# Performance work log

Measured on AMD Instinct MI355X. Metric: run time of the kernel, lower is better.

Reference implementation:

```python
import jax, jax.numpy as jnp
import numpy as np

N_EMBED = 1024
CUTOFFS = [20000, 60000, 180000]
N_VOCAB = 267735
BOUNDS = [0] + CUTOFFS + [N_VOCAB]            # cluster boundaries
N_EMBEDS = [1024, 256, 64, 16]                # n_embed / 4**i
N_TOK = 1024
N_CLUSTERS = len(CUTOFFS)                      # 3 tail clusters


def setup_inputs() -> dict:
    key = jax.random.key(0)
    ks = jax.random.split(key, 12)

    def w(k, shape):
        fan_in = shape[0]
        return (jax.random.normal(k, shape, jnp.float32) / np.sqrt(fan_in)).astype(jnp.float32)

    inp = {}
    inp["hidden"] = jax.random.normal(ks[0], (N_TOK, N_EMBED), jnp.float32)
    inp["target"] = jax.random.randint(ks[1], (N_TOK,), 0, N_VOCAB)
    # head: layers[0] = Linear(n_embed, cutoffs[0]); clusters = Linear(n_embed, n_clusters)
    inp["W_head"] = w(ks[2], (N_EMBED, BOUNDS[1]))
    inp["b_head"] = jnp.zeros((BOUNDS[1],), jnp.float32)
    inp["W_cluster"] = w(ks[3], (N_EMBED, N_CLUSTERS))
    inp["b_cluster"] = jnp.zeros((N_CLUSTERS,), jnp.float32)
    # tails: projections[i-1] = Linear(n_embed, n_embeds[i], bias=False); layers[i] = Linear(n_embeds[i], end-start)
    for i in range(1, N_CLUSTERS + 1):
        size = BOUNDS[i + 1] - BOUNDS[i]
        inp[f"W_proj{i}"] = w(ks[3 + 2 * i], (N_EMBED, N_EMBEDS[i]))
        inp[f"W_tail{i}"] = w(ks[4 + 2 * i], (N_EMBEDS[i], size))
        inp[f"b_tail{i}"] = jnp.zeros((size,), jnp.float32)
    return inp


def _adaptive_nll(hidden, target, W_head, b_head, W_cluster, b_cluster, tails):
    # head logits = [vocab cluster 0 | cluster logits], then log_softmax (matches torch.cat + log_softmax)
    head_logit = jnp.concatenate(
        [hidden @ W_head + b_head, hidden @ W_cluster + b_cluster], axis=1)  # [N, cut0 + n_clusters]
    head_lp = jax.nn.log_softmax(head_logit, axis=1)

    # cluster 0: logprob = head_lp[n, target]
    t0 = jnp.clip(target, 0, BOUNDS[1] - 1)
    lp0 = jnp.take_along_axis(head_lp, t0[:, None], axis=1)[:, 0]
    nll = jnp.where(target < BOUNDS[1], -lp0, jnp.zeros((), head_lp.dtype))

    # tail clusters i=1..3: logprob = head_lp[:, -i] + tail_log_softmax[n, target-start]
    for i, (Wp, Wt, bt) in enumerate(tails, start=1):
        start, end = BOUNDS[i], BOUNDS[i + 1]
        tail_lp = jax.nn.log_softmax((hidden @ Wp) @ Wt + bt, axis=1)  # [N, end-start]
        rel = jnp.clip(target - start, 0, end - start - 1)
        lp_i = head_lp[:, -i] + jnp.take_along_axis(tail_lp, rel[:, None], axis=1)[:, 0]
        in_bucket = (target >= start) & (target < end)
        nll = jnp.where(in_bucket, -lp_i, nll)
    return nll  # [N], per-token negative log-likelihood (keep_order=True semantics)


def reference(hidden, target, W_head, b_head, W_cluster, b_cluster,
              W_proj1, W_tail1, b_tail1,
              W_proj2, W_tail2, b_tail2,
              W_proj3, W_tail3, b_tail3):
    tails = [(W_proj1, W_tail1, b_tail1),
             (W_proj2, W_tail2, b_tail2),
             (W_proj3, W_tail3, b_tail3)]
    return _adaptive_nll(hidden, target, W_head, b_head, W_cluster, b_cluster, tails)
```

## Files before the change

kernel.cpp:

```cpp
#include <hip/hip_runtime.h>
#include <cstdint>
#include <cstddef>


typedef unsigned short u16;
typedef __attribute__((ext_vector_type(8))) __bf16 bf16x8;
typedef __attribute__((ext_vector_type(8))) u16 u16x8;
typedef __attribute__((ext_vector_type(4))) float f32x4;

#define AS1 __attribute__((address_space(1)))
#define AS3 __attribute__((address_space(3)))

__device__ __forceinline__ u16 f2bf(float f){
  union { float f; unsigned u; } v; v.f = f;
  unsigned r = v.u + 0x7fffu + ((v.u >> 16) & 1u);
  return (u16)(r >> 16);
}
__device__ __forceinline__ void glds16(const void* g, void* l){
  __builtin_amdgcn_global_load_lds((AS1 unsigned*)(uintptr_t)g,
                                   (AS3 unsigned*)(unsigned)(uintptr_t)l, 16, 0, 0);
}

__global__ void k_cvt_hidden(const float* __restrict__ h, u16* __restrict__ a0,
                             int* __restrict__ cnt, int* __restrict__ trel){
  int g = blockIdx.x * 256 + threadIdx.x;
  if (g < 4096) trel[g] = -1;
  if (g < 4) cnt[g] = 0;
  int i = g * 8;
  f32x4 v0 = *(const f32x4*)(h + i);
  f32x4 v1 = *(const f32x4*)(h + i + 4);
  u16x8 o;
  o[0]=f2bf(v0.x); o[1]=f2bf(v0.y); o[2]=f2bf(v0.z); o[3]=f2bf(v0.w);
  o[4]=f2bf(v1.x); o[5]=f2bf(v1.y); o[6]=f2bf(v1.z); o[7]=f2bf(v1.w);
  *(u16x8*)(a0 + i) = o;
}

__global__ void k_compact(const int* __restrict__ tgt, int* __restrict__ cnt,
                          int* __restrict__ idx1, int* __restrict__ idx2,
                          int* __restrict__ idx3, int* __restrict__ pos,
                          int* __restrict__ tr0, int* __restrict__ tr1,
                          int* __restrict__ tr2, int* __restrict__ tr3){
  int n = blockIdx.x * 256 + threadIdx.x;
  int t = tgt[n];
  int p = 0;
  tr0[n] = (t < 20000) ? t : -1;
  if (t >= 20000){
    int b = (t < 60000) ? 0 : (t < 180000 ? 1 : 2);
    p = atomicAdd(&cnt[b], 1);
    if (b == 0){ idx1[p] = n; tr1[p] = t - 20000; }
    else if (b == 1){ idx2[p] = n; tr2[p] = t - 60000; }
    else { idx3[p] = n; tr3[p] = t - 180000; }
  }
  pos[n] = p;
}

__global__ void k_gather(const int* __restrict__ cnt,
                         const int* __restrict__ idx1, const int* __restrict__ idx2,
                         const int* __restrict__ idx3,
                         const u16* __restrict__ A1, const u16* __restrict__ A2,
                         const u16* __restrict__ A3,
                         u16* __restrict__ A1c, u16* __restrict__ A2c,
                         u16* __restrict__ A3c){
  int u = blockIdx.x * 256 + threadIdx.x;
  const u16* src; u16* dst;
  if (u < 32768){
    int r = u >> 5, c = u & 31;
    if (r >= cnt[0]) return;
    src = A1 + (size_t)idx1[r] * 256 + c * 8;
    dst = A1c + (size_t)r * 256 + c * 8;
  } else if (u < 40960){
    int v = u - 32768; int r = v >> 3, c = v & 7;
    if (r >= cnt[1]) return;
    src = A2 + (size_t)idx2[r] * 64 + c * 8;
    dst = A2c + (size_t)r * 64 + c * 8;
  } else {
    int v = u - 40960; int r = v >> 2, c = v & 3;
    if (r >= cnt[2]) return;
    src = A3 + (size_t)idx3[r] * 32 + c * 8;
    dst = A3c + (size_t)r * 32 + c * 8;
  }
  *(u16x8*)dst = *(const u16x8*)src;
}

struct TJob { const float* W; u16* BT; int K, N, Kpad, nrows, nx, base, blk; };
struct TJobs { TJob j[8]; int nj; };

__global__ void k_transpose_multi(TJobs jobs){
  int id = blockIdx.x;
  int ji = 0;
  #pragma unroll
  for (int i = 1; i < 8; ++i)
    if (i < jobs.nj && id >= jobs.j[i].base) ji = i;
  TJob jb = jobs.j[ji];
  int local = id - jb.base;
  int bx = local % jb.nx;
  int by = local / jb.nx;

  __shared__ float t[64][65];
  const int n0 = bx * 64;
  const int k0 = by * 64;
  const bool al = (jb.N & 3) == 0;
  for (int i = threadIdx.x; i < 64*16; i += 256){
    int r = i >> 4, c4 = (i & 15) * 4;
    int k = k0 + r, n = n0 + c4;
    f32x4 v; v.x=0.f; v.y=0.f; v.z=0.f; v.w=0.f;
    if (k < jb.K){
      if (al && n + 3 < jb.N) v = *(const f32x4*)(jb.W + (size_t)k * jb.N + n);
      else { for (int q = 0; q < 4; ++q) if (n + q < jb.N) v[q] = jb.W[(size_t)k * jb.N + n + q]; }
    }
    t[r][c4] = v.x; t[r][c4+1] = v.y; t[r][c4+2] = v.z; t[r][c4+3] = v.w;
  }
  __syncthreads();
  for (int i = threadIdx.x; i < 64*8; i += 256){
    int rn = i >> 3, c8 = (i & 7) * 8;
    int n = n0 + rn;
    if (k0 + c8 < jb.Kpad && n < jb.nrows){
      u16x8 o;
      #pragma unroll
      for (int q = 0; q < 8; ++q) o[q] = f2bf(t[c8 + q][rn]);
      size_t off;
      if (jb.blk)
        off = (((size_t)(n >> 7) * (jb.Kpad >> 6) + (k0 >> 6)) * 128 + (n & 127)) * 64 + c8;
      else
        off = (size_t)n * jb.Kpad + k0 + c8;
      *(u16x8*)(jb.BT + off) = o;
    }
  }
}

__global__ __launch_bounds__(512)
void k_proj_gemm(const u16* __restrict__ A, const u16* __restrict__ BT,
                 const float* __restrict__ bc,
                 u16* __restrict__ A1, u16* __restrict__ A2,
                 u16* __restrict__ A3, float* __restrict__ cl)
{
  constexpr int BK = 64, K = 1024;
  __shared__ u16 As[256 * BK];
  __shared__ u16 Bs[128 * BK];
  const int tid  = threadIdx.x;
  const int lane = tid & 63, wid = tid >> 6;
  const int wm = wid & 3, wn = wid >> 2;
  const int l15 = lane & 15, l4 = lane >> 4;
  const int m0 = blockIdx.y * 256;
  const int n0 = blockIdx.x * 128;

  f32x4 acc[4][4];
  #pragma unroll
  for (int m = 0; m < 4; ++m)
    #pragma unroll
    for (int n = 0; n < 4; ++n){ acc[m][n].x=0.f; acc[m][n].y=0.f; acc[m][n].z=0.f; acc[m][n].w=0.f; }

  for (int kt = 0; kt < K / BK; ++kt){
    #pragma unroll
    for (int i = 0; i < 4; ++i){
      int c = wid * 4 + i;
      int row = c * 8 + lane / 8, kb = lane % 8;
      glds16((const char*)(A + (size_t)(m0 + row) * K + kt * BK) + kb * 16,
             (char*)As + c * 1024);
    }
    #pragma unroll
    for (int i = 0; i < 2; ++i){
      int c = wid * 2 + i;
      int row = c * 8 + lane / 8, kb = lane % 8;
      glds16((const char*)(BT + (size_t)(n0 + row) * K + kt * BK) + kb * 16,
             (char*)Bs + c * 1024);
    }
    __syncthreads();
    #pragma unroll
    for (int ks = 0; ks < 2; ++ks){
      bf16x8 af[4], bfr[4];
      #pragma unroll
      for (int m = 0; m < 4; ++m)
        af[m] = *(const bf16x8*)((const char*)As + (wm*64 + m*16 + l15) * (BK*2) + ks*64 + l4*16);
      #pragma unroll
      for (int n = 0; n < 4; ++n)
        bfr[n] = *(const bf16x8*)((const char*)Bs + (wn*64 + n*16 + l15) * (BK*2) + ks*64 + l4*16);
      #pragma unroll
      for (int m = 0; m < 4; ++m)
        #pragma unroll
        for (int n = 0; n < 4; ++n)
          acc[m][n] = __builtin_amdgcn_mfma_f32_16x16x32_bf16(af[m], bfr[n], acc[m][n], 0, 0, 0);
    }
    __syncthreads();
  }
  #pragma unroll
  for (int m = 0; m < 4; ++m)
    #pragma unroll
    for (int n = 0; n < 4; ++n)
      #pragma unroll
      for (int q = 0; q < 4; ++q){
        int c = n0 + wn*64 + n*16 + l15;
        int r = m0 + wm*64 + m*16 + l4*4 + q;
        float v = acc[m][n][q];
        if (c < 256)      A1[(size_t)r*256 + c] = f2bf(v);
        else if (c < 320) A2[(size_t)r*64 + (c-256)] = f2bf(v);
        else if (c < 336){ u16* p = A3 + (size_t)r*32 + (c-320);
                           p[0] = f2bf(v); p[16] = 0; }
        else if (c < 339) cl[(size_t)r*3 + (c-336)] = v + bc[c-336];
      }
}

__global__ __launch_bounds__(512)
void k_gemm_lse256(const u16* __restrict__ A, const u16* __restrict__ BT,
                   const float* __restrict__ bias, int K, int N,
                   float* __restrict__ P, int ntiles,
                   const int* __restrict__ cntp, int bucket,
                   const int* __restrict__ tgt_rel, const int* __restrict__ rowmap,
                   float* __restrict__ tl)
{
  constexpr int BK = 64;
  if (cntp && (int)(blockIdx.y * 256) >= cntp[bucket]) return;
  __shared__ u16 As[256 * BK];
  __shared__ u16 Bs[128 * BK];
  __shared__ float reds[2][256];
  __shared__ int trel_s[256];

  const int tid  = threadIdx.x;
  const int lane = tid & 63, wid = tid >> 6;
  const int wm = wid & 3, wn = wid >> 2;
  const int l15 = lane & 15, l4 = lane >> 4;
  const int m0 = blockIdx.y * 256;
  const int n0 = blockIdx.x * 128;
  const int srow = lane >> 3, skb = lane & 7;

  if (tid < 256) trel_s[tid] = tgt_rel[m0 + tid];

  f32x4 acc[4][4];
  #pragma unroll
  for (int m = 0; m < 4; ++m)
    #pragma unroll
    for (int n = 0; n < 4; ++n){ acc[m][n].x=0.f; acc[m][n].y=0.f; acc[m][n].z=0.f; acc[m][n].w=0.f; }

  const int ksteps = K / BK;
  for (int kt = 0; kt < ksteps; ++kt){
    #pragma unroll
    for (int i = 0; i < 4; ++i){
      int c = wid * 4 + i;
      int row = c * 8 + srow;
      int kbs = skb ^ (row & 7);
      glds16((const char*)(A + (size_t)(m0 + row) * K + kt * BK) + kbs * 16,
             (char*)As + c * 1024);
    }
    #pragma unroll
    for (int i = 0; i < 2; ++i){
      int c = wid * 2 + i;
      int row = c * 8 + srow;
      int kbs = skb ^ (row & 7);
      glds16((const char*)(BT + ((size_t)(blockIdx.x * ksteps + kt) * 128 + row) * 64) + kbs * 16,
             (char*)Bs + c * 1024);
    }
    __syncthreads();
    #pragma unroll
    for (int ks = 0; ks < 2; ++ks){
      bf16x8 af[4], bfr[4];
      #pragma unroll
      for (int m = 0; m < 4; ++m){
        int r = wm*64 + m*16 + l15;
        af[m] = *(const bf16x8*)((const char*)As + r*128 + (((ks*4 + l4) ^ (r & 7)) * 16));
      }
      #pragma unroll
      for (int n = 0; n < 4; ++n){
        int r = wn*64 + n*16 + l15;
        bfr[n] = *(const bf16x8*)((const char*)Bs + r*128 + (((ks*4 + l4) ^ (r & 7)) * 16));
      }
      #pragma unroll
      for (int m = 0; m < 4; ++m)
        #pragma unroll
        for (int n = 0; n < 4; ++n)
          acc[m][n] = __builtin_amdgcn_mfma_f32_16x16x32_bf16(af[m], bfr[n], acc[m][n], 0, 0, 0);
    }
    __syncthreads();
  }

  float bv[4]; bool val[4];
  #pragma unroll
  for (int n = 0; n < 4; ++n){
    int col = n0 + wn*64 + n*16 + l15;
    val[n] = col < N;
    bv[n] = val[n] ? bias[col] : 0.f;
  }
  #pragma unroll
  for (int m = 0; m < 4; ++m)
    #pragma unroll
    for (int q = 0; q < 4; ++q){
      int lrow = wm*64 + m*16 + l4*4 + q;
      int tr = trel_s[lrow];
      float Sl = 0.f;
      #pragma unroll
      for (int n = 0; n < 4; ++n){
        if (val[n]){
          float lg = acc[m][n][q] + bv[n];
          Sl += __expf(lg);
          int col = n0 + wn*64 + n*16 + l15;
          if (tr == col) tl[rowmap ? rowmap[m0 + lrow] : (m0 + lrow)] = lg;
        }
      }
      #pragma unroll
      for (int d = 1; d < 16; d <<= 1) Sl += __shfl_xor(Sl, d);
      if (l15 == 0) reds[wn][lrow] = Sl;
    }
  __syncthreads();
  if (wn == 0 && l15 == 0){
    #pragma unroll
    for (int m = 0; m < 4; ++m)
      #pragma unroll
      for (int q = 0; q < 4; ++q){
        int lrow = wm*64 + m*16 + l4*4 + q;
        P[(size_t)(m0 + lrow) * ntiles + blockIdx.x] = reds[0][lrow] + reds[1][lrow];
      }
  }
}

template<int NC, int BK>
__global__ __launch_bounds__(256)
void k_gemm_lse_s(const u16* __restrict__ A, const u16* __restrict__ BT,
                  const float* __restrict__ bias, int N,
                  float* __restrict__ P, int ntiles,
                  const int* __restrict__ cntp, int bucket,
                  const int* __restrict__ tgt_rel, const int* __restrict__ rowmap,
                  float* __restrict__ tl)
{
  constexpr int CH  = BK / 8;
  constexpr int LPR = CH;
  constexpr int RPC = 64 / LPR;
  constexpr int CPW = (128 * BK * 2 / 1024) / 4;
  const int m0 = blockIdx.y * 128;
  if (m0 >= cntp[bucket]) return;
  const int cg = blockIdx.x;

  __shared__ u16 As[128 * BK];
  __shared__ u16 Bs[2][128 * BK];
  __shared__ float reds[2][128];
  __shared__ int trel_s[128];

  const int tid  = threadIdx.x;
  const int lane = tid & 63, wid = tid >> 6;
  const int wm = wid & 1, wn = wid >> 1;
  const int l15 = lane & 15, l4 = lane >> 4;
  const int srow = lane / LPR, skb = lane % LPR;

  if (tid < 128) trel_s[tid] = tgt_rel[m0 + tid];

  #pragma unroll
  for (int i = 0; i < CPW; ++i){
    int c = wid * CPW + i;
    int row = c * RPC + srow;
    int kbs = skb ^ (row & (CH - 1));
    glds16((const char*)(A + (size_t)(m0 + row) * BK) + kbs * 16,
           (char*)As + c * 1024);
  }
  {
    int ci0 = cg * NC;
    if (ci0 < ntiles){
      #pragma unroll
      for (int i = 0; i < CPW; ++i){
        int c = wid * CPW + i;
        int row = c * RPC + srow;
        int kbs = skb ^ (row & (CH - 1));
        glds16((const char*)(BT + (size_t)(ci0*128 + row) * BK) + kbs * 16,
               (char*)Bs[0] + c * 1024);
      }
    }
  }
  __syncthreads();

  int buf = 0;
  for (int ct = 0; ct < NC; ++ct){
    int ci = cg * NC + ct;
    if (ci >= ntiles) break;
    if (ct + 1 < NC && ci + 1 < ntiles){
      #pragma unroll
      for (int i = 0; i < CPW; ++i){
        int c = wid * CPW + i;
        int row = c * RPC + srow;
        int kbs = skb ^ (row & (CH - 1));
        glds16((const char*)(BT + (size_t)((ci+1)*128 + row) * BK) + kbs * 16,
               (char*)Bs[buf ^ 1] + c * 1024);
      }
    }
    f32x4 acc[4][4];
    #pragma unroll
    for (int m = 0; m < 4; ++m)
      #pragma unroll
      for (int n = 0; n < 4; ++n){ acc[m][n].x=0.f; acc[m][n].y=0.f; acc[m][n].z=0.f; acc[m][n].w=0.f; }
    #pragma unroll
    for (int ks = 0; ks < BK / 32; ++ks){
      bf16x8 af[4], bfr[4];
      #pragma unroll
      for (int m = 0; m < 4; ++m){
        int r = wm*64 + m*16 + l15;
        af[m] = *(const bf16x8*)((const char*)As + r*(BK*2) + (((ks*4 + l4) ^ (r & (CH-1))) * 16));
      }
      #pragma unroll
      for (int n = 0; n < 4; ++n){
        int r = wn*64 + n*16 + l15;
        bfr[n] = *(const bf16x8*)((const char*)Bs[buf] + r*(BK*2) + (((ks*4 + l4) ^ (r & (CH-1))) * 16));
      }
      #pragma unroll
      for (int m = 0; m < 4; ++m)
        #pragma unroll
        for (int n = 0; n < 4; ++n)
          acc[m][n] = __builtin_amdgcn_mfma_f32_16x16x32_bf16(af[m], bfr[n], acc[m][n], 0, 0, 0);
    }
    const int n0 = ci * 128;
    float bv[4]; bool val[4];
    #pragma unroll
    for (int n = 0; n < 4; ++n){
      int col = n0 + wn*64 + n*16 + l15;
      val[n] = col < N;
      bv[n] = val[n] ? bias[col] : 0.f;
    }
    #pragma unroll
    for (int m = 0; m < 4; ++m)
      #pragma unroll
      for (int q = 0; q < 4; ++q){
        int lrow = wm*64 + m*16 + l4*4 + q;
        int tr = trel_s[lrow];
        float Sl = 0.f;
        #pragma unroll
        for (int n = 0; n < 4; ++n){
          if (val[n]){
            float lg = acc[m][n][q] + bv[n];
            Sl += __expf(lg);
            int col = n0 + wn*64 + n*16 + l15;
            if (tr == col) tl[rowmap[m0 + lrow]] = lg;
          }
        }
        #pragma unroll
        for (int d = 1; d < 16; d <<= 1) Sl += __shfl_xor(Sl, d);
        if (l15 == 0) reds[wn][lrow] = Sl;
      }
    __syncthreads();
    if (wn == 0 && l15 == 0){
      #pragma unroll
      for (int m = 0; m < 4; ++m)
        #pragma unroll
        for (int q = 0; q < 4; ++q){
          int lrow = wm*64 + m*16 + l4*4 + q;
          P[(size_t)(m0 + lrow) * ntiles + ci] = reds[0][lrow] + reds[1][lrow];
        }
    }
    __syncthreads();
    buf ^= 1;
  }
}

__global__ void k_finalize(const int* __restrict__ tgt, const float* __restrict__ P,
                           const float* __restrict__ cl, const float* __restrict__ tl,
                           const int* __restrict__ pos, float* __restrict__ out)
{
  const int NT0 = 157, NT1 = 313, NT2 = 938, NT3 = 686;
  int n = blockIdx.x * 4 + (threadIdx.x >> 6);
  int lane = threadIdx.x & 63;
  int t = tgt[n];

  float s = 0.f;
  const float* p0 = P + (size_t)n * NT0;
  for (int i = lane; i < NT0; i += 64) s += p0[i];
  if (lane < 3) s += __expf(cl[n*3 + lane]);
  #pragma unroll
  for (int d = 1; d < 64; d <<= 1) s += __shfl_xor(s, d);
  float lse_head = logf(s);

  float nll;
  if (t < 20000){
    nll = lse_head - tl[n];
  } else {
    int seg, nt; size_t base;
    if      (t <  60000){ seg = 1; nt = NT1; base = (size_t)1024 * NT0; }
    else if (t < 180000){ seg = 2; nt = NT2; base = (size_t)1024 * (NT0 + NT1); }
    else                { seg = 3; nt = NT3; base = (size_t)1024 * (NT0 + NT1 + NT2); }
    float s2 = 0.f;
    const float* ps = P + base + (size_t)pos[n] * nt;
    for (int i = lane; i < nt; i += 64) s2 += ps[i];
    #pragma unroll
    for (int d = 1; d < 64; d <<= 1) s2 += __shfl_xor(s2, d);
    float lse_t = logf(s2);
    nll = lse_head - cl[n*3 + (3 - seg)] + lse_t - tl[n];
  }
  if (lane == 0) out[n] = nll;
}

extern "C" void kernel_launch(void* const* d_in, const int* in_sizes, int n_in,
                              void* d_out, int out_size, void* d_ws, size_t ws_size,
                              hipStream_t stream)
{
  const float* hidden = (const float*)d_in[0];
  const int*   target = (const int*)d_in[1];
  const float* W_head = (const float*)d_in[2];
  const float* b_head = (const float*)d_in[3];
  const float* W_clu  = (const float*)d_in[4];
  const float* b_clu  = (const float*)d_in[5];
  const float* W_p1   = (const float*)d_in[6];
  const float* W_t1   = (const float*)d_in[7];
  const float* b_t1   = (const float*)d_in[8];
  const float* W_p2   = (const float*)d_in[9];
  const float* W_t2   = (const float*)d_in[10];
  const float* b_t2   = (const float*)d_in[11];
  const float* W_p3   = (const float*)d_in[12];
  const float* W_t3   = (const float*)d_in[13];
  const float* b_t3   = (const float*)d_in[14];
  float* out = (float*)d_out;

  char* ws = (char*)d_ws;
  u16*   A0  = (u16*)(ws + 0);
  u16*   A1  = (u16*)(ws + 2097152);
  u16*   A2  = (u16*)(ws + 2621440);
  u16*   A3  = (u16*)(ws + 2752512);
  float* cl  = (float*)(ws + 2883584);
  float* tl  = (float*)(ws + 2895872);
  float* P   = (float*)(ws + 2899968);
  u16*   BTp = (u16*)(ws + 2899968);
  u16*   BTh = (u16*)(ws + 11476992);
  int*   cnt  = (int*)(ws + 52633600);
  int*   idx1 = (int*)(ws + 52633856);
  int*   idx2 = (int*)(ws + 52637952);
  int*   idx3 = (int*)(ws + 52642048);
  int*   pos  = (int*)(ws + 52646144);
  u16*   A1c  = (u16*)(ws + 52650240);
  u16*   A2c  = (u16*)(ws + 53174528);
  u16*   A3c  = (u16*)(ws + 53305600);
  int*   tr0  = (int*)(ws + 53436672);
  int*   tr1  = (int*)(ws + 53440768);
  int*   tr2  = (int*)(ws + 53444864);
  int*   tr3  = (int*)(ws + 53448960);
  u16*   BT1  = (u16*)(ws + 53453056);
  u16*   BT2  = (u16*)(ws + 73965824);
  u16*   BT3  = (u16*)(ws + 89334016);
  const size_t needA = 95000000;
  const bool bigws = ws_size >= needA;

  float* P0  = P;
  float* Pp1 = P + (size_t)1024 * 157;
  float* Pp2 = P + (size_t)1024 * (157 + 313);
  float* Pp3 = P + (size_t)1024 * (157 + 313 + 938);

  k_cvt_hidden<<<512, 256, 0, stream>>>(hidden, A0, cnt, tr0);
  k_compact<<<4, 256, 0, stream>>>(target, cnt, idx1, idx2, idx3, pos,
                                   tr0, tr1, tr2, tr3);

  TJobs tj{}; int nb = 0;
  auto add = [&](const float* W, u16* B, int K, int N, int Kpad, int nrows, int blk){
    int nx = (nrows + 63) / 64;
    int ny = (Kpad + 63) / 64;
    tj.j[tj.nj++] = TJob{W, B, K, N, Kpad, nrows, nx, nb, blk};
    nb += nx * ny;
  };
  add(W_p1, BTp, 1024, 256, 1024, 256, 0);
  add(W_p2, BTp + (size_t)256*1024, 1024, 64, 1024, 64, 0);
  add(W_p3, BTp + (size_t)320*1024, 1024, 16, 1024, 16, 0);
  add(W_clu, BTp + (size_t)336*1024, 1024, 3, 1024, 64, 0);
  add(W_head, BTh, 1024, 20000, 1024, 20096, 1);
  if (bigws){
    add(W_t1, BT1, 256, 40000, 256, 40064, 1);
    add(W_t2, BT2, 64, 120000, 64, 120064, 0);
    add(W_t3, BT3, 16, 87735, 32, 87808, 0);
  }
  k_transpose_multi<<<nb, 256, 0, stream>>>(tj);

  k_proj_gemm<<<dim3(3, 4), 512, 0, stream>>>(A0, BTp, b_clu, A1, A2, A3, cl);
  k_gather<<<192, 256, 0, stream>>>(cnt, idx1, idx2, idx3, A1, A2, A3, A1c, A2c, A3c);

  k_gemm_lse256<<<dim3(157, 4), 512, 0, stream>>>(A0, BTh, b_head, 1024, 20000,
      P0, 157, nullptr, 0, tr0, nullptr, tl);

  if (bigws){
    k_gemm_lse256<<<dim3(313, 4), 512, 0, stream>>>(A1c, BT1, b_t1, 256, 40000,
        Pp1, 313, cnt, 0, tr1, idx1, tl);
    k_gemm_lse_s<4, 64><<<dim3(235, 8), 256, 0, stream>>>(A2c, BT2, b_t2, 120000,
        Pp2, 938, cnt, 1, tr2, idx2, tl);
    k_gemm_lse_s<4, 32><<<dim3(172, 8), 256, 0, stream>>>(A3c, BT3, b_t3, 87735,
        Pp3, 686, cnt, 2, tr3, idx3, tl);
  } else {
    TJobs s1{}; s1.nj = 1; s1.j[0] = TJob{W_t1, BTh, 256, 40000, 256, 40064, 626, 0, 1};
    k_transpose_multi<<<626*4, 256, 0, stream>>>(s1);
    k_gemm_lse256<<<dim3(313, 4), 512, 0, stream>>>(A1c, BTh, b_t1, 256, 40000,
        Pp1, 313, cnt, 0, tr1, idx1, tl);
    TJobs s2{}; s2.nj = 1; s2.j[0] = TJob{W_t2, BTh, 64, 120000, 64, 120064, 1876, 0, 0};
    k_transpose_multi<<<1876, 256, 0, stream>>>(s2);
    k_gemm_lse_s<4, 64><<<dim3(235, 8), 256, 0, stream>>>(A2c, BTh, b_t2, 120000,
        Pp2, 938, cnt, 1, tr2, idx2, tl);
    TJobs s3{}; s3.nj = 1; s3.j[0] = TJob{W_t3, BTh, 16, 87735, 32, 87808, 1372, 0, 0};
    k_transpose_multi<<<1372, 256, 0, stream>>>(s3);
    k_gemm_lse_s<4, 32><<<dim3(172, 8), 256, 0, stream>>>(A3c, BTh, b_t3, 87735,
        Pp3, 686, cnt, 2, tr3, idx3, tl);
  }

  k_finalize<<<256, 256, 0, stream>>>(target, P, cl, tl, pos, out);
}
```

Before: 274.3 us.

## Overlap head GEMM with tail weight transposes in a combined kernel

New measurement: 265.4 us. 1.03x faster.

```diff
diff --git a/kernel.cpp b/kernel.cpp
--- a/kernel.cpp
+++ b/kernel.cpp
@@ -15,6 +15,10 @@
   union { float f; unsigned u; } v; v.f = f;
   unsigned r = v.u + 0x7fffu + ((v.u >> 16) & 1u);
   return (u16)(r >> 16);
+}
+__device__ __forceinline__ float bf2f(u16 x){
+  union { unsigned u; float f; } v; v.u = ((unsigned)x) << 16;
+  return v.f;
 }
 __device__ __forceinline__ void glds16(const void* g, void* l){
   __builtin_amdgcn_global_load_lds((AS1 unsigned*)(uintptr_t)g,
@@ -85,8 +89,9 @@
 struct TJob { const float* W; u16* BT; int K, N, Kpad, nrows, nx, base, blk; };
 struct TJobs { TJob j[8]; int nj; };
 
-__global__ void k_transpose_multi(TJobs jobs){
-  int id = blockIdx.x;
+template<int TPB>
+__device__ __forceinline__ void transpose_tile(const TJobs& jobs, int id,
+                                               float (*t)[65], int tid){
   int ji = 0;
   #pragma unroll
   for (int i = 1; i < 8; ++i)
@@ -96,11 +101,10 @@
   int bx = local % jb.nx;
   int by = local / jb.nx;
 
-  __shared__ float t[64][65];
   const int n0 = bx * 64;
   const int k0 = by * 64;
   const bool al = (jb.N & 3) == 0;
-  for (int i = threadIdx.x; i < 64*16; i += 256){
+  for (int i = tid; i < 64*16; i += TPB){
     int r = i >> 4, c4 = (i & 15) * 4;
     int k = k0 + r, n = n0 + c4;
     f32x4 v; v.x=0.f; v.y=0.f; v.z=0.f; v.w=0.f;
@@ -111,7 +115,7 @@
     t[r][c4] = v.x; t[r][c4+1] = v.y; t[r][c4+2] = v.z; t[r][c4+3] = v.w;
   }
   __syncthreads();
-  for (int i = threadIdx.x; i < 64*8; i += 256){
+  for (int i = tid; i < 64*8; i += TPB){
     int rn = i >> 3, c8 = (i & 7) * 8;
     int n = n0 + rn;
     if (k0 + c8 < jb.Kpad && n < jb.nrows){
@@ -126,6 +130,11 @@
       *(u16x8*)(jb.BT + off) = o;
     }
   }
+}
+
+__global__ void k_transpose_multi(TJobs jobs){
+  __shared__ float t[64][65];
+  transpose_tile<256>(jobs, blockIdx.x, t, threadIdx.x);
 }
 
 __global__ __launch_bounds__(512)
@@ -200,6 +209,111 @@
       }
 }
 
+__device__ __forceinline__
+void gemm256_body(const u16* __restrict__ A, const u16* __restrict__ BT,
+                  const float* __restrict__ bias, int K, int N,
+                  float* __restrict__ P, int ntiles, int cb, int rb,
+                  const int* __restrict__ tgt_rel, const int* __restrict__ rowmap,
+                  float* __restrict__ tl,
+                  u16* As, u16* Bs, float* reds , int* trel_s)
+{
+  constexpr int BK = 64;
+  const int tid  = threadIdx.x;
+  const int lane = tid & 63, wid = tid >> 6;
+  const int wm = wid & 3, wn = wid >> 2;
+  const int l15 = lane & 15, l4 = lane >> 4;
+  const int m0 = rb * 256;
+  const int n0 = cb * 128;
+  const int srow = lane >> 3, skb = lane & 7;
+
+  if (tid < 256) trel_s[tid] = tgt_rel[m0 + tid];
+
+  f32x4 acc[4][4];
+  #pragma unroll
+  for (int m = 0; m < 4; ++m)
+    #pragma unroll
+    for (int n = 0; n < 4; ++n){ acc[m][n].x=0.f; acc[m][n].y=0.f; acc[m][n].z=0.f; acc[m][n].w=0.f; }
+
+  const int ksteps = K / BK;
+  for (int kt = 0; kt < ksteps; ++kt){
+    #pragma unroll
+    for (int i = 0; i < 4; ++i){
+      int c = wid * 4 + i;
+      int row = c * 8 + srow;
+      int kbs = skb ^ (row & 7);
+      glds16((const char*)(A + (size_t)(m0 + row) * K + kt * BK) + kbs * 16,
+             (char*)As + c * 1024);
+    }
+    #pragma unroll
+    for (int i = 0; i < 2; ++i){
+      int c = wid * 2 + i;
+      int row = c * 8 + srow;
+      int kbs = skb ^ (row & 7);
+      glds16((const char*)(BT + ((size_t)(cb * ksteps + kt) * 128 + row) * 64) + kbs * 16,
+             (char*)Bs + c * 1024);
+    }
+    __syncthreads();
+    #pragma unroll
+    for (int ks = 0; ks < 2; ++ks){
+      bf16x8 af[4], bfr[4];
+      #pragma unroll
+      for (int m = 0; m < 4; ++m){
+        int r = wm*64 + m*16 + l15;
+        af[m] = *(const bf16x8*)((const char*)As + r*128 + (((ks*4 + l4) ^ (r & 7)) * 16));
+      }
+      #pragma unroll
+      for (int n = 0; n < 4; ++n){
+        int r = wn*64 + n*16 + l15;
+        bfr[n] = *(const bf16x8*)((const char*)Bs + r*128 + (((ks*4 + l4) ^ (r & 7)) * 16));
+      }
+      #pragma unroll
+      for (int m = 0; m < 4; ++m)
+        #pragma unroll
+        for (int n = 0; n < 4; ++n)
+          acc[m][n] = __builtin_amdgcn_mfma_f32_16x16x32_bf16(af[m], bfr[n], acc[m][n], 0, 0, 0);
+    }
+    __syncthreads();
+  }
+
+  float bv[4]; bool val[4];
+  #pragma unroll
+  for (int n = 0; n < 4; ++n){
+    int col = n0 + wn*64 + n*16 + l15;
+    val[n] = col < N;
+    bv[n] = val[n] ? bias[col] : 0.f;
+  }
+  #pragma unroll
+  for (int m = 0; m < 4; ++m)
+    #pragma unroll
+    for (int q = 0; q < 4; ++q){
+      int lrow = wm*64 + m*16 + l4*4 + q;
+      int tr = trel_s[lrow];
+      float Sl = 0.f;
+      #pragma unroll
+      for (int n = 0; n < 4; ++n){
+        if (val[n]){
+          float lg = acc[m][n][q] + bv[n];
+          Sl += __expf(lg);
+          int col = n0 + wn*64 + n*16 + l15;
+          if (tr == col) tl[rowmap ? rowmap[m0 + lrow] : (m0 + lrow)] = lg;
+        }
+      }
+      #pragma unroll
+      for (int d = 1; d < 16; d <<= 1) Sl += __shfl_xor(Sl, d);
+      if (l15 == 0) reds[wn*256 + lrow] = Sl;
+    }
+  __syncthreads();
+  if (wn == 0 && l15 == 0){
+    #pragma unroll
+    for (int m = 0; m < 4; ++m)
+      #pragma unroll
+      for (int q = 0; q < 4; ++q){
+        int lrow = wm*64 + m*16 + l4*4 + q;
+        P[(size_t)(m0 + lrow) * ntiles + cb] = reds[lrow] + reds[256 + lrow];
+      }
+  }
+}
+
 __global__ __launch_bounds__(512)
 void k_gemm_lse256(const u16* __restrict__ A, const u16* __restrict__ BT,
                    const float* __restrict__ bias, int K, int N,
@@ -208,106 +322,33 @@
                    const int* __restrict__ tgt_rel, const int* __restrict__ rowmap,
                    float* __restrict__ tl)
 {
-  constexpr int BK = 64;
   if (cntp && (int)(blockIdx.y * 256) >= cntp[bucket]) return;
-  __shared__ u16 As[256 * BK];
-  __shared__ u16 Bs[128 * BK];
-  __shared__ float reds[2][256];
+  __shared__ u16 As[256 * 64];
+  __shared__ u16 Bs[128 * 64];
+  __shared__ float reds[2 * 256];
   __shared__ int trel_s[256];
-
-  const int tid  = threadIdx.x;
-  const int lane = tid & 63, wid = tid >> 6;
-  const int wm = wid & 3, wn = wid >> 2;
-  const int l15 = lane & 15, l4 = lane >> 4;
-  const int m0 = blockIdx.y * 256;
-  const int n0 = blockIdx.x * 128;
-  const int srow = lane >> 3, skb = lane & 7;
-
-  if (tid < 256) trel_s[tid] = tgt_rel[m0 + tid];
-
-  f32x4 acc[4][4];
-  #pragma unroll
-  for (int m = 0; m < 4; ++m)
-    #pragma unroll
-    for (int n = 0; n < 4; ++n){ acc[m][n].x=0.f; acc[m][n].y=0.f; acc[m][n].z=0.f; acc[m][n].w=0.f; }
-
-  const int ksteps = K / BK;
-  for (int kt = 0; kt < ksteps; ++kt){
-    #pragma unroll
-    for (int i = 0; i < 4; ++i){
-      int c = wid * 4 + i;
-      int row = c * 8 + srow;
-      int kbs = skb ^ (row & 7);
-      glds16((const char*)(A + (size_t)(m0 + row) * K + kt * BK) + kbs * 16,
-             (char*)As + c * 1024);
-    }
-    #pragma unroll
-    for (int i = 0; i < 2; ++i){
-      int c = wid * 2 + i;
-      int row = c * 8 + srow;
-      int kbs = skb ^ (row & 7);
-      glds16((const char*)(BT + ((size_t)(blockIdx.x * ksteps + kt) * 128 + row) * 64) + kbs * 16,
-             (char*)Bs + c * 1024);
-    }
-    __syncthreads();
-    #pragma unroll
-    for (int ks = 0; ks < 2; ++ks){
-      bf16x8 af[4], bfr[4];
-      #pragma unroll
-      for (int m = 0; m < 4; ++m){
-        int r = wm*64 + m*16 + l15;
-        af[m] = *(const bf16x8*)((const char*)As + r*128 + (((ks*4 + l4) ^ (r & 7)) * 16));
-      }
-      #pragma unroll
-      for (int n = 0; n < 4; ++n){
-        int r = wn*64 + n*16 + l15;
-        bfr[n] = *(const bf16x8*)((const char*)Bs + r*128 + (((ks*4 + l4) ^ (r & 7)) * 16));
-      }
-      #pragma unroll
-      for (int m = 0; m < 4; ++m)
-        #pragma unroll
-        for (int n = 0; n < 4; ++n)
-          acc[m][n] = __builtin_amdgcn_mfma_f32_16x16x32_bf16(af[m], bfr[n], acc[m][n], 0, 0, 0);
-    }
-    __syncthreads();
-  }
-
-  float bv[4]; bool val[4];
-  #pragma unroll
-  for (int n = 0; n < 4; ++n){
-    int col = n0 + wn*64 + n*16 + l15;
-    val[n] = col < N;
-    bv[n] = val[n] ? bias[col] : 0.f;
-  }
-  #pragma unroll
-  for (int m = 0; m < 4; ++m)
-    #pragma unroll
-    for (int q = 0; q < 4; ++q){
-      int lrow = wm*64 + m*16 + l4*4 + q;
-      int tr = trel_s[lrow];
-      float Sl = 0.f;
-      #pragma unroll
-      for (int n = 0; n < 4; ++n){
-        if (val[n]){
-          float lg = acc[m][n][q] + bv[n];
-          Sl += __expf(lg);
-          int col = n0 + wn*64 + n*16 + l15;
-          if (tr == col) tl[rowmap ? rowmap[m0 + lrow] : (m0 + lrow)] = lg;
-        }
-      }
-      #pragma unroll
-      for (int d = 1; d < 16; d <<= 1) Sl += __shfl_xor(Sl, d);
-      if (l15 == 0) reds[wn][lrow] = Sl;
-    }
-  __syncthreads();
-  if (wn == 0 && l15 == 0){
-    #pragma unroll
-    for (int m = 0; m < 4; ++m)
-      #pragma unroll
-      for (int q = 0; q < 4; ++q){
-        int lrow = wm*64 + m*16 + l4*4 + q;
-        P[(size_t)(m0 + lrow) * ntiles + blockIdx.x] = reds[0][lrow] + reds[1][lrow];
-      }
+  gemm256_body(A, BT, bias, K, N, P, ntiles, blockIdx.x, blockIdx.y,
+               tgt_rel, rowmap, tl, As, Bs, reds, trel_s);
+}
+
+__global__ __launch_bounds__(512)
+void k_mega(const u16* __restrict__ A, const u16* __restrict__ BT,
+            const float* __restrict__ bias, int ntiles,
+            float* __restrict__ P, const int* __restrict__ tgt_rel,
+            float* __restrict__ tl, int gb, TJobs tails)
+{
+  __shared__ __align__(16) char smem[52224];
+  if ((int)blockIdx.x < gb){
+    u16* As = (u16*)smem;
+    u16* Bs = (u16*)(smem + 32768);
+    float* reds = (float*)(smem + 49152);
+    int* trel_s = (int*)(smem + 51200);
+    gemm256_body(A, BT, bias, 1024, 20000, P, ntiles,
+                 blockIdx.x % ntiles, blockIdx.x / ntiles,
+                 tgt_rel, nullptr, tl, As, Bs, reds, trel_s);
+  } else {
+    float (*t)[65] = (float(*)[65])smem;
+    transpose_tile<512>(tails, blockIdx.x - gb, t, threadIdx.x);
   }
 }
 
@@ -539,32 +580,33 @@
   k_compact<<<4, 256, 0, stream>>>(target, cnt, idx1, idx2, idx3, pos,
                                    tr0, tr1, tr2, tr3);
 
-  TJobs tj{}; int nb = 0;
-  auto add = [&](const float* W, u16* B, int K, int N, int Kpad, int nrows, int blk){
+  auto addj = [](TJobs& tj, int& nb, const float* W, u16* B, int K, int N,
+                 int Kpad, int nrows, int blk){
     int nx = (nrows + 63) / 64;
     int ny = (Kpad + 63) / 64;
     tj.j[tj.nj++] = TJob{W, B, K, N, Kpad, nrows, nx, nb, blk};
     nb += nx * ny;
   };
-  add(W_p1, BTp, 1024, 256, 1024, 256, 0);
-  add(W_p2, BTp + (size_t)256*1024, 1024, 64, 1024, 64, 0);
-  add(W_p3, BTp + (size_t)320*1024, 1024, 16, 1024, 16, 0);
-  add(W_clu, BTp + (size_t)336*1024, 1024, 3, 1024, 64, 0);
-  add(W_head, BTh, 1024, 20000, 1024, 20096, 1);
+
   if (bigws){
-    add(W_t1, BT1, 256, 40000, 256, 40064, 1);
-    add(W_t2, BT2, 64, 120000, 64, 120064, 0);
-    add(W_t3, BT3, 16, 87735, 32, 87808, 0);
-  }
-  k_transpose_multi<<<nb, 256, 0, stream>>>(tj);
-
-  k_proj_gemm<<<dim3(3, 4), 512, 0, stream>>>(A0, BTp, b_clu, A1, A2, A3, cl);
-  k_gather<<<192, 256, 0, stream>>>(cnt, idx1, idx2, idx3, A1, A2, A3, A1c, A2c, A3c);
-
-  k_gemm_lse256<<<dim3(157, 4), 512, 0, stream>>>(A0, BTh, b_head, 1024, 20000,
-      P0, 157, nullptr, 0, tr0, nullptr, tl);
-
-  if (bigws){
+    TJobs tj{}; int nb = 0;
+    addj(tj, nb, W_p1, BTp, 1024, 256, 1024, 256, 0);
+    addj(tj, nb, W_p2, BTp + (size_t)256*1024, 1024, 64, 1024, 64, 0);
+    addj(tj, nb, W_p3, BTp + (size_t)320*1024, 1024, 16, 1024, 16, 0);
+    addj(tj, nb, W_clu, BTp + (size_t)336*1024, 1024, 3, 1024, 64, 0);
+    addj(tj, nb, W_head, BTh, 1024, 20000, 1024, 20096, 1);
+    k_transpose_multi<<<nb, 256, 0, stream>>>(tj);
+
+    k_proj_gemm<<<dim3(3, 4), 512, 0, stream>>>(A0, BTp, b_clu, A1, A2, A3, cl);
+    k_gather<<<192, 256, 0, stream>>>(cnt, idx1, idx2, idx3, A1, A2, A3, A1c, A2c, A3c);
+
+    TJobs tt{}; int nbT = 0;
+    addj(tt, nbT, W_t1, BT1, 256, 40000, 256, 40064, 1);
+    addj(tt, nbT, W_t2, BT2, 64, 120000, 64, 120064, 0);
+    addj(tt, nbT, W_t3, BT3, 16, 87735, 32, 87808, 0);
+    const int gb = 157 * 4;
+    k_mega<<<gb + nbT, 512, 0, stream>>>(A0, BTh, b_head, 157, P0, tr0, tl, gb, tt);
+
     k_gemm_lse256<<<dim3(313, 4), 512, 0, stream>>>(A1c, BT1, b_t1, 256, 40000,
         Pp1, 313, cnt, 0, tr1, idx1, tl);
     k_gemm_lse_s<4, 64><<<dim3(235, 8), 256, 0, stream>>>(A2c, BT2, b_t2, 120000,
@@ -572,16 +614,33 @@
     k_gemm_lse_s<4, 32><<<dim3(172, 8), 256, 0, stream>>>(A3c, BT3, b_t3, 87735,
         Pp3, 686, cnt, 2, tr3, idx3, tl);
   } else {
-    TJobs s1{}; s1.nj = 1; s1.j[0] = TJob{W_t1, BTh, 256, 40000, 256, 40064, 626, 0, 1};
-    k_transpose_multi<<<626*4, 256, 0, stream>>>(s1);
+    TJobs tj{}; int nb = 0;
+    addj(tj, nb, W_p1, BTp, 1024, 256, 1024, 256, 0);
+    addj(tj, nb, W_p2, BTp + (size_t)256*1024, 1024, 64, 1024, 64, 0);
+    addj(tj, nb, W_p3, BTp + (size_t)320*1024, 1024, 16, 1024, 16, 0);
+    addj(tj, nb, W_clu, BTp + (size_t)336*1024, 1024, 3, 1024, 64, 0);
+    addj(tj, nb, W_head, BTh, 1024, 20000, 1024, 20096, 1);
+    k_transpose_multi<<<nb, 256, 0, stream>>>(tj);
+
+    k_proj_gemm<<<dim3(3, 4), 512, 0, stream>>>(A0, BTp, b_clu, A1, A2, A3, cl);
+    k_gather<<<192, 256, 0, stream>>>(cnt, idx1, idx2, idx3, A1, A2, A3, A1c, A2c, A3c);
+
+    k_gemm_lse256<<<dim3(157, 4), 512, 0, stream>>>(A0, BTh, b_head, 1024, 20000,
+        P0, 157, nullptr, 0, tr0, nullptr, tl);
+
+    TJobs s1{}; int n1 = 0;
+    addj(s1, n1, W_t1, BTh, 256, 40000, 256, 40064, 1);
+    k_transpose_multi<<<n1, 256, 0, stream>>>(s1);
     k_gemm_lse256<<<dim3(313, 4), 512, 0, stream>>>(A1c, BTh, b_t1, 256, 40000,
         Pp1, 313, cnt, 0, tr1, idx1, tl);
-    TJobs s2{}; s2.nj = 1; s2.j[0] = TJob{W_t2, BTh, 64, 120000, 64, 120064, 1876, 0, 0};
-    k_transpose_multi<<<1876, 256, 0, stream>>>(s2);
+    TJobs s2{}; int n2 = 0;
+    addj(s2, n2, W_t2, BTh, 64, 120000, 64, 120064, 0);
+    k_transpose_multi<<<n2, 256, 0, stream>>>(s2);
     k_gemm_lse_s<4, 64><<<dim3(235, 8), 256, 0, stream>>>(A2c, BTh, b_t2, 120000,
         Pp2, 938, cnt, 1, tr2, idx2, tl);
-    TJobs s3{}; s3.nj = 1; s3.j[0] = TJob{W_t3, BTh, 16, 87735, 32, 87808, 1372, 0, 0};
-    k_transpose_multi<<<1372, 256, 0, stream>>>(s3);
+    TJobs s3{}; int n3 = 0;
+    addj(s3, n3, W_t3, BTh, 16, 87735, 32, 87808, 0);
+    k_transpose_multi<<<n3, 256, 0, stream>>>(s3);
     k_gemm_lse_s<4, 32><<<dim3(172, 8), 256, 0, stream>>>(A3c, BTh, b_t3, 87735,
         Pp3, 686, cnt, 2, tr3, idx3, tl);
   }
```
